# Performance work log

Hardware: AMD Instinct MI355X
Metric: run time of the kernel (lower is better)

The kernel has to match this reference:

```python
import jax, jax.numpy as jnp
import numpy as np

N_NODES = 100000
N_EDGES = 800000
D = 256
OUT = 1

def _glorot(key, shape):
    fan_in, fan_out = shape[1], shape[0]
    lim = np.sqrt(6.0 / (fan_in + fan_out)).astype(np.float32)
    return jax.random.uniform(key, shape, jnp.float32, -lim, lim)

def setup_inputs() -> dict:
    key = jax.random.key(0)
    ks = jax.random.split(key, 12)
    x = jax.random.normal(ks[0], (N_NODES, D), jnp.float32)
    edge_index = jax.random.randint(ks[1], (2, N_EDGES), 0, N_NODES, jnp.int64)
    return {
        "x": x,
        "edge_index": edge_index,
        # SAGEConv: lin_l acts on aggregated neighbors (has bias), lin_r on root (no bias)
        "W_l": _glorot(ks[2], (256, D)),
        "b_l": jnp.zeros((256,), jnp.float32),
        "W_r": _glorot(ks[3], (256, D)),
        # MLP
        "W1": _glorot(ks[4], (128, 256)),
        "b1": jnp.zeros((128,), jnp.float32),
        "W2": _glorot(ks[5], (32, 128)),
        "b2": jnp.zeros((32,), jnp.float32),
        "W3": _glorot(ks[6], (OUT, 32)),
        "b3": jnp.zeros((OUT,), jnp.float32),
    }

def reference(x, edge_index, W_l, b_l, W_r, W1, b1, W2, b2, W3, b3):
    src, dst = edge_index[0], edge_index[1]
    # mean aggregation of neighbor (source) features at destination nodes
    msg = x[src]                                            # [E, D]
    agg = jax.ops.segment_sum(msg, dst, num_segments=N_NODES)   # [N, D]
    cnt = jax.ops.segment_sum(jnp.ones((edge_index.shape[1],), x.dtype), dst,
                              num_segments=N_NODES)          # [N]
    mean = agg / jnp.maximum(cnt, 1.0)[:, None]
    # SAGEConv: lin_l(mean_neigh) + lin_r(x)
    conv = mean @ W_l.T + b_l + x @ W_r.T                   # [N, 256]
    out = jax.nn.relu(conv)
    h = out + x                                              # residual
    h = jax.nn.relu(h @ W1.T + b1)
    h = jax.nn.relu(h @ W2.T + b2)
    return h @ W3.T + b3                                     # [N, OUT]
```

## Files before the change

kernel.cpp:

```cpp
#include <hip/hip_runtime.h>
#include <cstddef>

#define NN 100000
#define NE 800000
#define DD 256
#define CAP 32
#define NSLICE 8
#define SLICEW 12500
#define ECH 8192

typedef unsigned short u16;
typedef __bf16 bf8_t __attribute__((ext_vector_type(8)));
typedef float f32x4 __attribute__((ext_vector_type(4)));
typedef u16 u16x8 __attribute__((ext_vector_type(8)));

__device__ __forceinline__ float bf2f(u16 u) {
    union { unsigned int i; float f; } v; v.i = ((unsigned int)u) << 16; return v.f;
}
__device__ __forceinline__ u16 f2bf(float f) {
    union { float f; unsigned int i; } v; v.f = f;
    unsigned int x = v.i;
    unsigned int r = (x + 0x7FFFu + ((x >> 16) & 1u)) >> 16;
    return (u16)r;
}

__device__ __forceinline__ void bar_lds() {
    asm volatile("s_waitcnt lgkmcnt(0)" ::: "memory");
    __builtin_amdgcn_s_barrier();
    asm volatile("" ::: "memory");
}

__global__ void GNNActor_23192823398472_kernel() {}

__device__ __forceinline__ float ldwf(const void* p, int i, int f32) {
    return f32 ? ((const float*)p)[i] : bf2f(((const u16*)p)[i]);
}

__global__ void k_prep(const u16* __restrict__ x, const int* __restrict__ ei,
                       int* __restrict__ flags, int4* __restrict__ z4, int nz4,
                       const void* __restrict__ Wl, const void* __restrict__ Wr,
                       const void* __restrict__ W1, const void* __restrict__ W2,
                       const void* __restrict__ W3, const void* __restrict__ bl,
                       const void* __restrict__ b1, const void* __restrict__ b2,
                       const void* __restrict__ b3, u16* __restrict__ pk,
                       float* __restrict__ pb) {
    int nzb = (nz4 + 255) / 256;
    if ((int)blockIdx.x < nzb) {
        int i = blockIdx.x * 256 + threadIdx.x;
        if (i < nz4) z4[i] = (int4){0, 0, 0, 0};
        if (blockIdx.x == 0 && threadIdx.x < 64) {
            int lane = threadIdx.x;
            int big = 0;
            for (int k = lane; k < 4096; k += 64) {
                u16 u = x[k];
                if (((u >> 7) & 0xFF) >= 140) ++big;
            }
            #pragma unroll
            for (int off = 32; off; off >>= 1) big += __shfl_down(big, off, 64);
            int bad = 0;
            for (int k = lane; k < 128; k += 64) bad |= (ei[2 * k + 1] != 0) ? 1 : 0;
            unsigned long long anybad = __ballot(bad);
            if (lane == 0) {
                flags[0] = (big > 64) ? 1 : 0;
                flags[1] = anybad ? 0 : 1;
            }
        }
        return;
    }
    __shared__ int s_f32;
    if (threadIdx.x < 64) {
        int lane = threadIdx.x;
        int big = 0;
        for (int k = lane; k < 4096; k += 64) {
            u16 u = x[k];
            if (((u >> 7) & 0xFF) >= 140) ++big;
        }
        #pragma unroll
        for (int off = 32; off; off >>= 1) big += __shfl_down(big, off, 64);
        if (lane == 0) s_f32 = (big > 64) ? 1 : 0;
    }
    __syncthreads();
    int f32 = s_f32;
    int id = (blockIdx.x - nzb) * 256 + threadIdx.x;
    if (id < 16384) {
        int lr = id & 15, lq = (id >> 4) & 3, c = (id >> 6) & 15, ctg = id >> 10;
        int n = ctg * 16 + lr;
        int k = (c & 7) * 32 + lq * 8;
        const void* W = (c < 8) ? Wl : Wr;
        u16x8 o;
        #pragma unroll
        for (int j = 0; j < 8; ++j) o[j] = f2bf(ldwf(W, n * DD + k + j, f32));
        *(u16x8*)&pk[id * 8] = o;
    } else if (id < 20480) {
        int id2 = id - 16384;
        int lr = id2 & 15, lq = (id2 >> 4) & 3, c = (id2 >> 6) & 7, wv = id2 >> 9;
        int n = wv * 16 + lr;
        u16x8 o;
        #pragma unroll
        for (int j = 0; j < 8; ++j) o[j] = f2bf(ldwf(W1, n * DD + c * 32 + lq * 8 + j, f32));
        *(u16x8*)&pk[131072 + id2 * 8] = o;
    } else if (id < 20992) {
        int id2 = id - 20480;
        int lr = id2 & 15, lq = (id2 >> 4) & 3, c = (id2 >> 6) & 3, wv = id2 >> 8;
        int n = wv * 16 + lr;
        u16x8 o;
        #pragma unroll
        for (int j = 0; j < 8; ++j) o[j] = f2bf(ldwf(W2, n * 128 + c * 32 + lq * 8 + j, f32));
        *(u16x8*)&pk[163840 + id2 * 8] = o;
    } else if (id < 21441) {
        int j = id - 20992;
        float v;
        if (j < 256)      v = ldwf(bl, j, f32);
        else if (j < 384) v = ldwf(b1, j - 256, f32);
        else if (j < 416) v = ldwf(b2, j - 384, f32);
        else if (j == 416) v = ldwf(b3, 0, f32);
        else              v = ldwf(W3, j - 417, f32);
        pb[j] = v;
    }
}

__launch_bounds__(256)
__global__ void k_scatter(const int* __restrict__ ei, int* __restrict__ cnt_i,
                          int* __restrict__ elist, const int* __restrict__ flags) {
    int chunk = blockIdx.x >> 3, slice = blockIdx.x & 7;
    int lo = slice * SLICEW, hi = lo + SLICEW;
    int i64 = flags[1];
    int base = chunk * ECH;
    #pragma unroll 1
    for (int k = 0; k < ECH / 1024; ++k) {
        int e0 = base + k * 1024 + threadIdx.x * 4;
        if (e0 >= NE) continue;
        int d0, d1, d2, d3;
        if (i64) {
            int4 a = *(const int4*)&ei[2 * NE + 2 * e0];
            int4 b = *(const int4*)&ei[2 * NE + 2 * e0 + 4];
            d0 = a.x; d1 = a.z; d2 = b.x; d3 = b.z;
        } else {
            int4 a = *(const int4*)&ei[NE + e0];
            d0 = a.x; d1 = a.y; d2 = a.z; d3 = a.w;
        }
        bool h0 = (d0 >= lo) & (d0 < hi);
        bool h1 = (d1 >= lo) & (d1 < hi);
        bool h2 = (d2 >= lo) & (d2 < hi);
        bool h3 = (d3 >= lo) & (d3 < hi);
        if (h0 | h1 | h2 | h3) {
            int s0, s1, s2, s3;
            if (i64) {
                int4 p = *(const int4*)&ei[2 * e0];
                int4 q = *(const int4*)&ei[2 * e0 + 4];
                s0 = p.x; s1 = p.z; s2 = q.x; s3 = q.z;
            } else {
                int4 p = *(const int4*)&ei[e0];
                s0 = p.x; s1 = p.y; s2 = p.z; s3 = p.w;
            }
            if (h0) { int p0 = atomicAdd(&cnt_i[d0], 1); if (p0 < CAP) elist[d0 * CAP + p0] = s0; }
            if (h1) { int p1 = atomicAdd(&cnt_i[d1], 1); if (p1 < CAP) elist[d1 * CAP + p1] = s1; }
            if (h2) { int p2 = atomicAdd(&cnt_i[d2], 1); if (p2 < CAP) elist[d2 * CAP + p2] = s2; }
            if (h3) { int p3 = atomicAdd(&cnt_i[d3], 1); if (p3 < CAP) elist[d3 * CAP + p3] = s3; }
        }
    }
}

#define SMS 264
#define SH1 136
#define SH2 40

template <int F32>
__device__ __forceinline__ void fused_body(
        const int* __restrict__ cnt_i, const int* __restrict__ elist,
        const void* __restrict__ xv,
        const u16* __restrict__ pk, const float* __restrict__ pb,
        void* __restrict__ outv, char* smem) {
    u16* s_mean = (u16*)smem;
    u16* s_x    = (u16*)(smem + 16896);
    u16* s_h    = (u16*)smem;
    u16* s_h1   = (u16*)(smem + 16896);
    u16* s_h2   = (u16*)smem;

    int t = threadIdx.x;
    int node0 = blockIdx.x * 32;
    int wv = t >> 6, lane = t & 63;
    int lq = lane >> 4, lr = lane & 15;
    int half = lane >> 5, li = lane & 31;
    int fo = lq * 128 + lr * 8;

    int ibase = (node0 + wv * 4) * CAP;
    int ridx0 = elist[ibase + lane];
    int ridx1 = elist[ibase + 64 + lane];
    int creg  = cnt_i[node0 + wv * 4 + (lane & 3)];

    int r0_ = t >> 5, k0_ = (t & 31) << 3;
    u16x8 hx0, hx1;
    if (F32) {
        const float* p0 = (const float*)xv + (size_t)(node0 + r0_) * DD + k0_;
        const float* p1 = (const float*)xv + (size_t)(node0 + 16 + r0_) * DD + k0_;
        float4 fa = *(const float4*)p0, fb = *(const float4*)(p0 + 4);
        float4 fc = *(const float4*)p1, fd = *(const float4*)(p1 + 4);
        hx0[0]=f2bf(fa.x); hx0[1]=f2bf(fa.y); hx0[2]=f2bf(fa.z); hx0[3]=f2bf(fa.w);
        hx0[4]=f2bf(fb.x); hx0[5]=f2bf(fb.y); hx0[6]=f2bf(fb.z); hx0[7]=f2bf(fb.w);
        hx1[0]=f2bf(fc.x); hx1[1]=f2bf(fc.y); hx1[2]=f2bf(fc.z); hx1[3]=f2bf(fc.w);
        hx1[4]=f2bf(fd.x); hx1[5]=f2bf(fd.y); hx1[6]=f2bf(fd.z); hx1[7]=f2bf(fd.w);
    } else {
        hx0 = *(const u16x8*)((const u16*)xv + (size_t)(node0 + r0_) * DD + k0_);
        hx1 = *(const u16x8*)((const u16*)xv + (size_t)(node0 + 16 + r0_) * DD + k0_);
    }

    #pragma unroll
    for (int q = 0; q < 4; ++q) {
        int cnt = __shfl(creg, q, 64);
        int m = cnt < CAP ? cnt : CAP;
        float a0=0.f,a1=0.f,a2=0.f,a3=0.f,a4=0.f,a5=0.f,a6=0.f,a7=0.f;
        #pragma unroll
        for (int B = 0; B < 2; ++B) {
            if (B * 16 < m) {
                u16x8 u[8]; float4 fA[8], fB[8];
                #pragma unroll
                for (int g = 0; g < 8; ++g) {
                    if (B * 16 + 2 * g < m) {
                        int j = B * 16 + 2 * g + half;
                        int jj = (j < m) ? j : 0;
                        int sl = __shfl(q < 2 ? ridx0 : ridx1, (q & 1) * 32 + jj, 64);
                        if (F32) {
                            const float* p = (const float*)xv + (size_t)sl * DD + li * 8;
                            fA[g] = *(const float4*)p;
                            fB[g] = *(const float4*)(p + 4);
                        } else {
                            u[g] = *(const u16x8*)((const u16*)xv + (size_t)sl * DD + li * 8);
                        }
                    }
                }
                #pragma unroll
                for (int g = 0; g < 8; ++g) {
                    if (B * 16 + 2 * g < m) {
                        float mg = (B * 16 + 2 * g + half < m) ? 1.f : 0.f;
                        if (F32) {
                            a0 = fmaf(mg, fA[g].x, a0); a1 = fmaf(mg, fA[g].y, a1);
                            a2 = fmaf(mg, fA[g].z, a2); a3 = fmaf(mg, fA[g].w, a3);
                            a4 = fmaf(mg, fB[g].x, a4); a5 = fmaf(mg, fB[g].y, a5);
                            a6 = fmaf(mg, fB[g].z, a6); a7 = fmaf(mg, fB[g].w, a7);
                        } else {
                            a0 = fmaf(mg, bf2f(u[g][0]), a0); a1 = fmaf(mg, bf2f(u[g][1]), a1);
                            a2 = fmaf(mg, bf2f(u[g][2]), a2); a3 = fmaf(mg, bf2f(u[g][3]), a3);
                            a4 = fmaf(mg, bf2f(u[g][4]), a4); a5 = fmaf(mg, bf2f(u[g][5]), a5);
                            a6 = fmaf(mg, bf2f(u[g][6]), a6); a7 = fmaf(mg, bf2f(u[g][7]), a7);
                        }
                    }
                }
            }
        }
        a0 += __shfl_xor(a0, 32, 64); a1 += __shfl_xor(a1, 32, 64);
        a2 += __shfl_xor(a2, 32, 64); a3 += __shfl_xor(a3, 32, 64);
        a4 += __shfl_xor(a4, 32, 64); a5 += __shfl_xor(a5, 32, 64);
        a6 += __shfl_xor(a6, 32, 64); a7 += __shfl_xor(a7, 32, 64);
        if (lane < 32) {
            float inv = 1.f / fmaxf((float)cnt, 1.f);
            u16x8 o;
            o[0]=f2bf(a0*inv); o[1]=f2bf(a1*inv); o[2]=f2bf(a2*inv); o[3]=f2bf(a3*inv);
            o[4]=f2bf(a4*inv); o[5]=f2bf(a5*inv); o[6]=f2bf(a6*inv); o[7]=f2bf(a7*inv);
            *(u16x8*)&s_mean[(wv * 4 + q) * SMS + li * 8] = o;
        }
    }

    const u16* pk1 = pk + 131072;
    const u16* pk2 = pk + 163840;
    int ctg0 = wv * 2, ctg1 = ctg0 + 1;
    #define LWC(ctg, c) (*(const bf8_t*)&pk[((ctg) * 16 + (c)) * 512 + fo])

    bf8_t w0[16], w1[16];
    #pragma unroll
    for (int c = 0; c < 4; ++c) { w0[c] = LWC(ctg0, c); w1[c] = LWC(ctg1, c); }

    *(u16x8*)&s_x[r0_ * SMS + k0_] = hx0;
    *(u16x8*)&s_x[(16 + r0_) * SMS + k0_] = hx1;

    bar_lds();

    f32x4 acc00 = (f32x4){0.f,0.f,0.f,0.f}, acc10 = (f32x4){0.f,0.f,0.f,0.f};
    f32x4 acc01 = (f32x4){0.f,0.f,0.f,0.f}, acc11 = (f32x4){0.f,0.f,0.f,0.f};

    #pragma unroll
    for (int c = 0; c < 16; ++c) {
        if (c < 12) { w0[c + 4] = LWC(ctg0, c + 4); w1[c + 4] = LWC(ctg1, c + 4); }
        const u16* ab = (c < 8) ? s_mean : s_x;
        int co = (c & 7) * 32 + lq * 8;
        bf8_t a0 = *(const bf8_t*)&ab[lr * SMS + co];
        bf8_t a1 = *(const bf8_t*)&ab[(16 + lr) * SMS + co];
        acc00 = __builtin_amdgcn_mfma_f32_16x16x32_bf16(a0, w0[c], acc00, 0, 0, 0);
        acc10 = __builtin_amdgcn_mfma_f32_16x16x32_bf16(a1, w0[c], acc10, 0, 0, 0);
        acc01 = __builtin_amdgcn_mfma_f32_16x16x32_bf16(a0, w1[c], acc01, 0, 0, 0);
        acc11 = __builtin_amdgcn_mfma_f32_16x16x32_bf16(a1, w1[c], acc11, 0, 0, 0);
    }

    bf8_t v1[8];
    #pragma unroll
    for (int c = 0; c < 8; ++c) v1[c] = *(const bf8_t*)&pk1[(wv * 8 + c) * 512 + fo];

    bar_lds();

    #pragma unroll
    for (int ct = 0; ct < 2; ++ct) {
        int n = (wv * 2 + ct) * 16 + lr;
        float bb = pb[n];
        const f32x4* ac0 = ct ? &acc01 : &acc00;
        const f32x4* ac1 = ct ? &acc11 : &acc10;
        #pragma unroll
        for (int i = 0; i < 4; ++i) {
            int m0 = lq * 4 + i;
            s_h[m0 * SMS + n] = f2bf(fmaxf((*ac0)[i] + bb, 0.f) + bf2f(s_x[m0 * SMS + n]));
            int m1 = 16 + lq * 4 + i;
            s_h[m1 * SMS + n] = f2bf(fmaxf((*ac1)[i] + bb, 0.f) + bf2f(s_x[m1 * SMS + n]));
        }
    }
    bar_lds();

    {
        f32x4 a1c0 = (f32x4){0.f,0.f,0.f,0.f}, a1c1 = (f32x4){0.f,0.f,0.f,0.f};
        int n = wv * 16 + lr;
        #pragma unroll
        for (int c = 0; c < 8; ++c) {
            bf8_t a0 = *(const bf8_t*)&s_h[lr * SMS + c * 32 + lq * 8];
            bf8_t a1 = *(const bf8_t*)&s_h[(16 + lr) * SMS + c * 32 + lq * 8];
            a1c0 = __builtin_amdgcn_mfma_f32_16x16x32_bf16(a0, v1[c], a1c0, 0, 0, 0);
            a1c1 = __builtin_amdgcn_mfma_f32_16x16x32_bf16(a1, v1[c], a1c1, 0, 0, 0);
        }
        bf8_t v2[4];
        if (wv < 2) {
            #pragma unroll
            for (int c = 0; c < 4; ++c) v2[c] = *(const bf8_t*)&pk2[(wv * 4 + c) * 512 + fo];
        }
        float bb = pb[256 + n];
        #pragma unroll
        for (int i = 0; i < 4; ++i) {
            int m0 = lq * 4 + i;
            s_h1[m0 * SH1 + n] = f2bf(fmaxf(a1c0[i] + bb, 0.f));
            int m1 = 16 + lq * 4 + i;
            s_h1[m1 * SH1 + n] = f2bf(fmaxf(a1c1[i] + bb, 0.f));
        }
        bar_lds();

        if (wv < 2) {
            f32x4 a2c0 = (f32x4){0.f,0.f,0.f,0.f}, a2c1 = (f32x4){0.f,0.f,0.f,0.f};
            #pragma unroll
            for (int c = 0; c < 4; ++c) {
                bf8_t a0 = *(const bf8_t*)&s_h1[lr * SH1 + c * 32 + lq * 8];
                bf8_t a1 = *(const bf8_t*)&s_h1[(16 + lr) * SH1 + c * 32 + lq * 8];
                a2c0 = __builtin_amdgcn_mfma_f32_16x16x32_bf16(a0, v2[c], a2c0, 0, 0, 0);
                a2c1 = __builtin_amdgcn_mfma_f32_16x16x32_bf16(a1, v2[c], a2c1, 0, 0, 0);
            }
            float bb2 = pb[384 + n];
            #pragma unroll
            for (int i = 0; i < 4; ++i) {
                int m0 = lq * 4 + i;
                s_h2[m0 * SH2 + n] = f2bf(fmaxf(a2c0[i] + bb2, 0.f));
                int m1 = 16 + lq * 4 + i;
                s_h2[m1 * SH2 + n] = f2bf(fmaxf(a2c1[i] + bb2, 0.f));
            }
        }
    }
    bar_lds();

    if (t < 32) {
        float a3 = pb[416];
        #pragma unroll
        for (int k = 0; k < 32; ++k)
            a3 += bf2f(s_h2[t * SH2 + k]) * pb[417 + k];
        if (F32) ((float*)outv)[node0 + t] = a3;
        else     ((u16*)outv)[node0 + t]   = f2bf(a3);
    }
    #undef LWC
}

__launch_bounds__(512, 4)
__global__ void k_fused(const int* __restrict__ cnt_i, const int* __restrict__ elist,
                        const void* __restrict__ xv,
                        const u16* __restrict__ pk, const float* __restrict__ pb,
                        void* __restrict__ outv, const int* __restrict__ flags) {
    __shared__ __align__(16) char smem[33792];
    if (flags[0]) fused_body<1>(cnt_i, elist, xv, pk, pb, outv, smem);
    else          fused_body<0>(cnt_i, elist, xv, pk, pb, outv, smem);
}

extern "C" void kernel_launch(void* const* d_in, const int* in_sizes, int n_in,
                              void* d_out, int out_size, void* d_ws, size_t ws_size,
                              hipStream_t stream) {
    const u16* x  = (const u16*)d_in[0];
    const int* ei = (const int*)d_in[1];
    const void* Wl = d_in[2];
    const void* bl = d_in[3];
    const void* Wr = d_in[4];
    const void* W1 = d_in[5];
    const void* b1 = d_in[6];
    const void* W2 = d_in[7];
    const void* b2 = d_in[8];
    const void* W3 = d_in[9];
    const void* b3 = d_in[10];

    int* flags = (int*)d_ws;
    int* cnt_i = flags + 256;
    int* elist = cnt_i + NN;
    u16* pk    = (u16*)(elist + (size_t)NN * CAP);
    float* pb  = (float*)(pk + 167936);

    int nz4 = NN / 4;
    int nzb = (nz4 + 255) / 256;
    int nchunk = (NE + ECH - 1) / ECH;
    k_prep<<<nzb + 84, 256, 0, stream>>>(x, ei, flags, (int4*)cnt_i, nz4,
                                         Wl, Wr, W1, W2, W3, bl, b1, b2, b3, pk, pb);
    k_scatter<<<nchunk * NSLICE, 256, 0, stream>>>(ei, cnt_i, elist, flags);
    k_fused<<<NN / 32, 512, 0, stream>>>(cnt_i, elist, (const void*)x, pk, pb,
                                         d_out, flags);
}
```

Measured before the change: 348.9 us.

## Pad per-node counters to 128B stride and scatter edges in one pass

Replaces the sliced scatter, which re-read the edge list once per destination slice for eight slices, with a single pass in which each thread handles four edges and issues four independent atomics. Each per-node counter is padded to a 32-int stride so every atomic lands on its own cache line, which is meant to avoid contention between neighbouring nodes. In exchange the counter array grows 32-fold, so the zeroing work in the prep kernel grows to about 12.8 MB, and the fused kernel reads the counts with a strided gather.

```diff
diff --git a/kernel.cpp b/kernel.cpp
--- a/kernel.cpp
+++ b/kernel.cpp
@@ -5,9 +5,7 @@
 #define NE 800000
 #define DD 256
 #define CAP 32
-#define NSLICE 8
-#define SLICEW 12500
-#define ECH 8192
+#define CSTRIDE 32
 
 typedef unsigned short u16;
 typedef __bf16 bf8_t __attribute__((ext_vector_type(8)));
@@ -120,45 +118,32 @@
 }
 
 __launch_bounds__(256)
-__global__ void k_scatter(const int* __restrict__ ei, int* __restrict__ cnt_i,
+__global__ void k_scatter(const int* __restrict__ ei, int* __restrict__ cnt_p,
                           int* __restrict__ elist, const int* __restrict__ flags) {
-    int chunk = blockIdx.x >> 3, slice = blockIdx.x & 7;
-    int lo = slice * SLICEW, hi = lo + SLICEW;
-    int i64 = flags[1];
-    int base = chunk * ECH;
-    #pragma unroll 1
-    for (int k = 0; k < ECH / 1024; ++k) {
-        int e0 = base + k * 1024 + threadIdx.x * 4;
-        if (e0 >= NE) continue;
-        int d0, d1, d2, d3;
-        if (i64) {
-            int4 a = *(const int4*)&ei[2 * NE + 2 * e0];
-            int4 b = *(const int4*)&ei[2 * NE + 2 * e0 + 4];
-            d0 = a.x; d1 = a.z; d2 = b.x; d3 = b.z;
-        } else {
-            int4 a = *(const int4*)&ei[NE + e0];
-            d0 = a.x; d1 = a.y; d2 = a.z; d3 = a.w;
-        }
-        bool h0 = (d0 >= lo) & (d0 < hi);
-        bool h1 = (d1 >= lo) & (d1 < hi);
-        bool h2 = (d2 >= lo) & (d2 < hi);
-        bool h3 = (d3 >= lo) & (d3 < hi);
-        if (h0 | h1 | h2 | h3) {
-            int s0, s1, s2, s3;
-            if (i64) {
-                int4 p = *(const int4*)&ei[2 * e0];
-                int4 q = *(const int4*)&ei[2 * e0 + 4];
-                s0 = p.x; s1 = p.z; s2 = q.x; s3 = q.z;
-            } else {
-                int4 p = *(const int4*)&ei[e0];
-                s0 = p.x; s1 = p.y; s2 = p.z; s3 = p.w;
-            }
-            if (h0) { int p0 = atomicAdd(&cnt_i[d0], 1); if (p0 < CAP) elist[d0 * CAP + p0] = s0; }
-            if (h1) { int p1 = atomicAdd(&cnt_i[d1], 1); if (p1 < CAP) elist[d1 * CAP + p1] = s1; }
-            if (h2) { int p2 = atomicAdd(&cnt_i[d2], 1); if (p2 < CAP) elist[d2 * CAP + p2] = s2; }
-            if (h3) { int p3 = atomicAdd(&cnt_i[d3], 1); if (p3 < CAP) elist[d3 * CAP + p3] = s3; }
-        }
-    }
+    int e0 = (blockIdx.x * blockDim.x + threadIdx.x) * 4;
+    if (e0 >= NE) return;
+    int d0, d1, d2, d3, s0, s1, s2, s3;
+    if (flags[1]) {
+        int4 a = *(const int4*)&ei[2 * NE + 2 * e0];
+        int4 b = *(const int4*)&ei[2 * NE + 2 * e0 + 4];
+        d0 = a.x; d1 = a.z; d2 = b.x; d3 = b.z;
+        int4 p = *(const int4*)&ei[2 * e0];
+        int4 q = *(const int4*)&ei[2 * e0 + 4];
+        s0 = p.x; s1 = p.z; s2 = q.x; s3 = q.z;
+    } else {
+        int4 a = *(const int4*)&ei[NE + e0];
+        d0 = a.x; d1 = a.y; d2 = a.z; d3 = a.w;
+        int4 p = *(const int4*)&ei[e0];
+        s0 = p.x; s1 = p.y; s2 = p.z; s3 = p.w;
+    }
+    int p0 = atomicAdd(&cnt_p[d0 * CSTRIDE], 1);
+    int p1 = atomicAdd(&cnt_p[d1 * CSTRIDE], 1);
+    int p2 = atomicAdd(&cnt_p[d2 * CSTRIDE], 1);
+    int p3 = atomicAdd(&cnt_p[d3 * CSTRIDE], 1);
+    if (p0 < CAP) elist[d0 * CAP + p0] = s0;
+    if (p1 < CAP) elist[d1 * CAP + p1] = s1;
+    if (p2 < CAP) elist[d2 * CAP + p2] = s2;
+    if (p3 < CAP) elist[d3 * CAP + p3] = s3;
 }
 
 #define SMS 264
@@ -167,7 +152,7 @@
 
 template <int F32>
 __device__ __forceinline__ void fused_body(
-        const int* __restrict__ cnt_i, const int* __restrict__ elist,
+        const int* __restrict__ cnt_p, const int* __restrict__ elist,
         const void* __restrict__ xv,
         const u16* __restrict__ pk, const float* __restrict__ pb,
         void* __restrict__ outv, char* smem) {
@@ -187,7 +172,7 @@
     int ibase = (node0 + wv * 4) * CAP;
     int ridx0 = elist[ibase + lane];
     int ridx1 = elist[ibase + 64 + lane];
-    int creg  = cnt_i[node0 + wv * 4 + (lane & 3)];
+    int creg  = cnt_p[(node0 + wv * 4 + (lane & 3)) * CSTRIDE];
 
     int r0_ = t >> 5, k0_ = (t & 31) << 3;
     u16x8 hx0, hx1;
@@ -371,13 +356,13 @@
 }
 
 __launch_bounds__(512, 4)
-__global__ void k_fused(const int* __restrict__ cnt_i, const int* __restrict__ elist,
+__global__ void k_fused(const int* __restrict__ cnt_p, const int* __restrict__ elist,
                         const void* __restrict__ xv,
                         const u16* __restrict__ pk, const float* __restrict__ pb,
                         void* __restrict__ outv, const int* __restrict__ flags) {
     __shared__ __align__(16) char smem[33792];
-    if (flags[0]) fused_body<1>(cnt_i, elist, xv, pk, pb, outv, smem);
-    else          fused_body<0>(cnt_i, elist, xv, pk, pb, outv, smem);
+    if (flags[0]) fused_body<1>(cnt_p, elist, xv, pk, pb, outv, smem);
+    else          fused_body<0>(cnt_p, elist, xv, pk, pb, outv, smem);
 }
 
 extern "C" void kernel_launch(void* const* d_in, const int* in_sizes, int n_in,
@@ -396,17 +381,16 @@
     const void* b3 = d_in[10];
 
     int* flags = (int*)d_ws;
-    int* cnt_i = flags + 256;
-    int* elist = cnt_i + NN;
+    int* cnt_p = flags + 256;
+    int* elist = cnt_p + (size_t)NN * CSTRIDE;
     u16* pk    = (u16*)(elist + (size_t)NN * CAP);
     float* pb  = (float*)(pk + 167936);
 
-    int nz4 = NN / 4;
+    int nz4 = NN * CSTRIDE / 4;
     int nzb = (nz4 + 255) / 256;
-    int nchunk = (NE + ECH - 1) / ECH;
-    k_prep<<<nzb + 84, 256, 0, stream>>>(x, ei, flags, (int4*)cnt_i, nz4,
+    k_prep<<<nzb + 84, 256, 0, stream>>>(x, ei, flags, (int4*)cnt_p, nz4,
                                          Wl, Wr, W1, W2, W3, bl, b1, b2, b3, pk, pb);
-    k_scatter<<<nchunk * NSLICE, 256, 0, stream>>>(ei, cnt_i, elist, flags);
-    k_fused<<<NN / 32, 512, 0, stream>>>(cnt_i, elist, (const void*)x, pk, pb,
+    k_scatter<<<(NE / 4 + 255) / 256, 256, 0, stream>>>(ei, cnt_p, elist, flags);
+    k_fused<<<NN / 32, 512, 0, stream>>>(cnt_p, elist, (const void*)x, pk, pb,
                                          d_out, flags);
 }
```

After: 359.5 us. 3.0% more time.
